# Kernel optimization log

Hardware: AMD Instinct MI355X
Metric: run time of the kernel (lower is better)

## Reference

```python
import jax, jax.numpy as jnp
import numpy as np

B, S, D = 2, 1024, 1024
L, E, F = 2, 8, 2048


def setup_inputs() -> dict:
    key = jax.random.key(0)
    kx, kp, k1, k2 = jax.random.split(key, 4)
    x = jax.random.normal(kx, (B, S, D), dtype=jnp.float32)
    # prototypes scaled so dot products are O(1), keeping softmax well-behaved
    protos = jax.random.normal(kp, (L, E, D), dtype=jnp.float32) / np.sqrt(D)
    W1 = jax.random.normal(k1, (L, E, D, F), dtype=jnp.float32) * 0.02
    W2 = jax.random.normal(k2, (L, E, F, D), dtype=jnp.float32) * 0.02
    return {"x": x, "protos": protos, "W1": W1, "W2": W2, "k": 2}


def _route(x, protos_l, k):
    # expert_mapping: abs(dot(prototype, input)) per expert, keep top-k, rest -> -inf, softmax
    scores = jnp.abs(jnp.einsum("bsd,ed->bse", x, protos_l))  # [B,S,E]
    topv, _ = jax.lax.top_k(scores, k)
    thresh = topv[..., -1:]  # k-th largest per token
    masked = jnp.where(scores >= thresh, scores, -jnp.inf)
    return jax.nn.softmax(masked, axis=-1)  # [B,S,E]


def reference(x, protos, W1, W2, k):
    n_layers = protos.shape[0]
    for l in range(n_layers):  # fixed small layer loop
        w = _route(x, protos[l], k)  # [B,S,E]
        h = jax.nn.relu(jnp.einsum("bsd,edf->bsef", x, W1[l]))  # [B,S,E,F]
        y = jnp.einsum("bsef,efd,bse->bsd", h, W2[l], w)  # weighted expert mix
        x = x + y
    return x
```

## Files before the change

### kernel.cpp

```cpp
#include <hip/hip_runtime.h>
#include <hip/hip_bf16.h>
#include <cstdint>

#define T_TOKENS 2048
#define DDIM 1024
#define FDIM 2048
#define NEXP 8
#define NLAYER 2
#define BMPAD 64
#define RMAX 4608
#define RALLOC 4736

#define ATILE_EL 2048
#define BTILE_EL 4096

typedef unsigned short u16;
typedef short bf16x8 __attribute__((ext_vector_type(8)));
typedef u16 u16x8 __attribute__((ext_vector_type(8)));
typedef u16 u16x4v __attribute__((ext_vector_type(4)));
typedef float f32x4 __attribute__((ext_vector_type(4)));

__device__ __forceinline__ u16 bf16_rn(float f) {
  unsigned u = __builtin_bit_cast(unsigned, f);
  u += 0x7fffu + ((u >> 16) & 1u);
  return (u16)(u >> 16);
}
__device__ __forceinline__ float bf16_f(u16 h) {
  unsigned u = ((unsigned)h) << 16;
  return __builtin_bit_cast(float, u);
}

__device__ __forceinline__ void gl16(const void* g, void* l) {
  __builtin_amdgcn_global_load_lds((const __attribute__((address_space(1))) void*)g,
                                   (__attribute__((address_space(3))) void*)l, 16, 0, 0);
}

__global__ __launch_bounds__(256) void route_kernel(
    const float* __restrict__ x, const float* __restrict__ protos,
    int* __restrict__ eid, float* __restrict__ wgt) {
  const int t = blockIdx.x;
  const int tid = threadIdx.x;
  const float* xr = x + (size_t)t * DDIM;
  __shared__ float red[NEXP][256];
  float acc[NEXP];
#pragma unroll
  for (int e = 0; e < NEXP; ++e) acc[e] = 0.f;
  for (int d = tid; d < DDIM; d += 256) {
    float xv = xr[d];
#pragma unroll
    for (int e = 0; e < NEXP; ++e) acc[e] += xv * protos[e * DDIM + d];
  }
#pragma unroll
  for (int e = 0; e < NEXP; ++e) red[e][tid] = acc[e];
  __syncthreads();
  for (int s = 128; s > 0; s >>= 1) {
    if (tid < s) {
#pragma unroll
      for (int e = 0; e < NEXP; ++e) red[e][tid] += red[e][tid + s];
    }
    __syncthreads();
  }
  if (tid == 0) {
    float m1 = -1.f, m2 = -1.f;
    int i1 = 0, i2 = 0;
#pragma unroll
    for (int e = 0; e < NEXP; ++e) {
      float s = fabsf(red[e][0]);
      if (s > m1) { m2 = m1; i2 = i1; m1 = s; i1 = e; }
      else if (s > m2) { m2 = s; i2 = e; }
    }
    float e2 = __expf(m2 - m1);
    float z = 1.f + e2;
    eid[t * 2] = i1;
    eid[t * 2 + 1] = i2;
    wgt[t * 2] = 1.f / z;
    wgt[t * 2 + 1] = e2 / z;
  }
}

__global__ __launch_bounds__(256) void compact_kernel(
    const int* __restrict__ eid, int* __restrict__ cnt, int* __restrict__ offp,
    int* __restrict__ row2token, int* __restrict__ pos) {
  __shared__ int lcnt[NEXP][256];
  __shared__ int s_off[NEXP], s_tot[NEXP];
  const int tid = threadIdx.x;
  const int base = tid * 16;

  int my[16];
#pragma unroll
  for (int i = 0; i < 4; ++i)
    *(int4*)&my[i * 4] = *(const int4*)(eid + base + i * 4);

#pragma unroll
  for (int e = 0; e < NEXP; ++e) {
    int c = 0;
#pragma unroll
    for (int i = 0; i < 16; ++i) c += (my[i] == e) ? 1 : 0;
    lcnt[e][tid] = c;
  }

  for (int r = tid; r < RMAX; r += 256) row2token[r] = -1;
  __syncthreads();

  if (tid < NEXP) {
    int run = 0;
    for (int i = 0; i < 256; ++i) {
      int v = lcnt[tid][i];
      lcnt[tid][i] = run;
      run += v;
    }
    s_tot[tid] = run;
  }
  __syncthreads();
  if (tid == 0) {
    int o = 0;
    for (int e = 0; e < NEXP; ++e) {
      s_off[e] = o;
      o += (s_tot[e] + BMPAD - 1) & ~(BMPAD - 1);
    }
  }
  __syncthreads();

  int myoff[NEXP];
#pragma unroll
  for (int e = 0; e < NEXP; ++e) myoff[e] = s_off[e] + lcnt[e][tid];
#pragma unroll
  for (int i = 0; i < 16; ++i) {
    int r = 0;
#pragma unroll
    for (int e = 0; e < NEXP; ++e) r = (my[i] == e) ? myoff[e] : r;
    row2token[r] = (base + i) >> 1;
    pos[base + i] = r;
#pragma unroll
    for (int e = 0; e < NEXP; ++e) myoff[e] += (my[i] == e) ? 1 : 0;
  }

  if (tid < NEXP) {
    cnt[tid] = s_tot[tid];
    offp[tid] = s_off[tid];
  }
}

__global__ __launch_bounds__(256) void gather_kernel(
    const float* __restrict__ x, const int* __restrict__ row2token,
    u16* __restrict__ Ahi, u16* __restrict__ Alo) {
  const int r = blockIdx.x;
  const int t = row2token[r];
  const int c = threadIdx.x * 4;
  float4 v = make_float4(0.f, 0.f, 0.f, 0.f);
  if (t >= 0) v = *(const float4*)(x + (size_t)t * DDIM + c);
  float vv[4] = {v.x, v.y, v.z, v.w};
  u16x4v hi, lo;
#pragma unroll
  for (int i = 0; i < 4; ++i) {
    u16 h = bf16_rn(vv[i]);
    hi[i] = h;
    lo[i] = bf16_rn(vv[i] - bf16_f(h));
  }
  const size_t el = ((size_t)(r >> 6) * (DDIM >> 5) + (c >> 5)) * ATILE_EL +
                    (size_t)(((c >> 3) & 3) * 64 + (r & 63)) * 8 + (c & 7);
  *(u16x4v*)(Ahi + el) = hi;
  *(u16x4v*)(Alo + el) = lo;
}

template <bool LO>
__global__ __launch_bounds__(256) void wconv_kernel(
    const float* __restrict__ W, u16* __restrict__ Hi, u16* __restrict__ Lo,
    int K, int N) {
  const int e = blockIdx.z, nb = blockIdx.x, kb = blockIdx.y;
  const float* Wp = W + ((size_t)e * K + (size_t)kb * 32) * N + nb * 128;
  __shared__ float tile[32][129];
  const int t = threadIdx.x;
#pragma unroll
  for (int i = 0; i < 4; ++i) {
    const int f4 = i * 256 + t;
    const int kr = f4 >> 5;
    const int c4 = (f4 & 31) * 4;
    float4 v = *(const float4*)(Wp + (size_t)kr * N + c4);
    *(float4*)&tile[kr][c4] = v;
  }
  __syncthreads();
  const size_t tb = (((size_t)e * (N >> 7) + nb) * (K >> 5) + kb) * BTILE_EL;
#pragma unroll
  for (int j = 0; j < 2; ++j) {
    const int cid = j * 256 + t;
    const int n = cid & 127, ksel = cid >> 7;
    u16x8 hv, lv;
#pragma unroll
    for (int i = 0; i < 8; ++i) {
      float f = tile[ksel * 8 + i][n];
      u16 h = bf16_rn(f);
      hv[i] = h;
      if (LO) lv[i] = bf16_rn(f - bf16_f(h));
    }
    *(u16x8*)(Hi + tb + (size_t)cid * 8) = hv;
    if (LO) *(u16x8*)(Lo + tb + (size_t)cid * 8) = lv;
  }
}

template <bool RELU, bool SPLIT, int OUTMODE, int SKF>
__global__ __launch_bounds__(256, SPLIT ? 2 : 4) void gemm_mfma(
    const u16* __restrict__ Ahi, const u16* __restrict__ Alo,
    const u16* __restrict__ Bhi, const u16* __restrict__ Blo,
    u16* __restrict__ OutHi, u16* __restrict__ OutLo, float* __restrict__ OutF,
    const int* __restrict__ cnt, const int* __restrict__ offp, int K, int N) {
  const int z = blockIdx.z;
  const int e = z / SKF, sk = z % SKF;
  const int cp = (cnt[e] + 63) & ~63;
  if ((int)(blockIdx.y * 128) >= cp) return;
  const int row0 = offp[e] + blockIdx.y * 128;
  const int rend = offp[e] + cp;
  const int n0 = blockIdx.x * 128;
  const int nkb = K >> 5;
  const int kbN = nkb / SKF;
  const int kb0 = sk * kbN;

  constexpr int BUF_EL = SPLIT ? 16384 : 8192;
  __shared__ u16 lds[2 * BUF_EL];

  const int tid = threadIdx.x;
  const int lane = tid & 63;
  const int wid = tid >> 6;
  const int wr = wid >> 1, wc = wid & 1;
  const int lr = lane & 15, kg = lane >> 4;
  const int lo16 = lane << 4;

  f32x4 acc[4][4];
#pragma unroll
  for (int i = 0; i < 4; ++i)
#pragma unroll
    for (int j = 0; j < 4; ++j)
#pragma unroll
      for (int r = 0; r < 4; ++r) acc[i][j][r] = 0.f;

  const int at0 = row0 >> 6;
  const size_t bbase = ((size_t)e * (N >> 7) + (n0 >> 7)) * nkb;

  auto STAGE = [&](int kb, int b) {
    char* d = (char*)(lds + b * BUF_EL);
    if constexpr (SPLIT) {
      if (wid == 0) {
#pragma unroll
        for (int t = 0; t < 2; ++t) {
          const char* g = (const char*)(Ahi + ((size_t)(at0 + t) * nkb + kb) * ATILE_EL);
#pragma unroll
          for (int i = 0; i < 4; ++i) gl16(g + i * 1024 + lo16, d + t * 4096 + i * 1024);
        }
      } else if (wid == 1) {
#pragma unroll
        for (int t = 0; t < 2; ++t) {
          const char* g = (const char*)(Alo + ((size_t)(at0 + t) * nkb + kb) * ATILE_EL);
#pragma unroll
          for (int i = 0; i < 4; ++i) gl16(g + i * 1024 + lo16, d + 8192 + t * 4096 + i * 1024);
        }
      } else if (wid == 2) {
        const char* g = (const char*)(Bhi + (bbase + kb) * BTILE_EL);
#pragma unroll
        for (int i = 0; i < 8; ++i) gl16(g + i * 1024 + lo16, d + 16384 + i * 1024);
      } else {
        const char* g = (const char*)(Blo + (bbase + kb) * BTILE_EL);
#pragma unroll
        for (int i = 0; i < 8; ++i) gl16(g + i * 1024 + lo16, d + 24576 + i * 1024);
      }
    } else {
      if (wid < 2) {
        const char* g = (const char*)(Ahi + ((size_t)(at0 + wid) * nkb + kb) * ATILE_EL);
#pragma unroll
        for (int i = 0; i < 4; ++i) gl16(g + i * 1024 + lo16, d + wid * 4096 + i * 1024);
      } else {
        const char* g = (const char*)(Bhi + (bbase + kb) * BTILE_EL) + (wid - 2) * 4096;
#pragma unroll
        for (int i = 0; i < 4; ++i) gl16(g + i * 1024 + lo16, d + 8192 + (wid - 2) * 4096 + i * 1024);
      }
    }
  };

  STAGE(kb0, 0);
  __syncthreads();

  int cur = 0;
  for (int kb = kb0; kb < kb0 + kbN; ++kb) {
    if (kb + 1 < kb0 + kbN) STAGE(kb + 1, cur ^ 1);

    const u16* buf = lds + cur * BUF_EL;
    const u16* AsH = buf + wr * 2048;
    const u16* BsH = buf + (SPLIT ? 8192 : 4096);
    const int arow = (kg * 64 + lr) * 8;
    const int bcol = (kg * 128 + wc * 64 + lr) * 8;

    bf16x8 ah[4], bh[4];
#pragma unroll
    for (int i = 0; i < 4; ++i) ah[i] = *(const bf16x8*)&AsH[arow + i * 128];
#pragma unroll
    for (int j = 0; j < 4; ++j) bh[j] = *(const bf16x8*)&BsH[bcol + j * 128];
#pragma unroll
    for (int i = 0; i < 4; ++i)
#pragma unroll
      for (int j = 0; j < 4; ++j)
        acc[i][j] = __builtin_amdgcn_mfma_f32_16x16x32_bf16(ah[i], bh[j], acc[i][j], 0, 0, 0);

    if constexpr (SPLIT) {
      const u16* AsL = buf + 4096 + wr * 2048;
      const u16* BsL = buf + 12288;
      bf16x8 bl[4];
#pragma unroll
      for (int j = 0; j < 4; ++j) bl[j] = *(const bf16x8*)&BsL[bcol + j * 128];
#pragma unroll
      for (int i = 0; i < 4; ++i)
#pragma unroll
        for (int j = 0; j < 4; ++j)
          acc[i][j] = __builtin_amdgcn_mfma_f32_16x16x32_bf16(ah[i], bl[j], acc[i][j], 0, 0, 0);
      bf16x8 al[4];
#pragma unroll
      for (int i = 0; i < 4; ++i) al[i] = *(const bf16x8*)&AsL[arow + i * 128];
#pragma unroll
      for (int i = 0; i < 4; ++i)
#pragma unroll
        for (int j = 0; j < 4; ++j)
          acc[i][j] = __builtin_amdgcn_mfma_f32_16x16x32_bf16(al[i], bh[j], acc[i][j], 0, 0, 0);
    }
    __syncthreads();
    cur ^= 1;
  }

  const int nkbO = N >> 5;
#pragma unroll
  for (int i = 0; i < 4; ++i) {
#pragma unroll
    for (int j = 0; j < 4; ++j) {
      const int Cj = n0 + wc * 64 + j * 16 + lr;
      f32x4 v = acc[i][j];
#pragma unroll
      for (int r = 0; r < 4; ++r) {
        const int R = row0 + wr * 64 + i * 16 + kg * 4 + r;
        if (R >= rend) continue;
        float f = v[r];
        if (RELU) f = fmaxf(f, 0.f);
        if constexpr (OUTMODE == 0) {
          OutF[((size_t)sk * RALLOC + R) * N + Cj] = f;
        } else {
          const size_t el = ((size_t)(R >> 6) * nkbO + (Cj >> 5)) * ATILE_EL +
                            (size_t)(((Cj >> 3) & 3) * 64 + (R & 63)) * 8 + (Cj & 7);
          u16 h = bf16_rn(f);
          OutHi[el] = h;
          if constexpr (OUTMODE == 1) OutLo[el] = bf16_rn(f - bf16_f(h));
        }
      }
    }
  }
}

__global__ __launch_bounds__(256) void apply_kernel(
    const float* __restrict__ part, const int* __restrict__ pos,
    const float* __restrict__ wgt, float* __restrict__ x) {
  const int t = blockIdx.x;
  const int c = threadIdx.x * 4;
  const int p0 = pos[t * 2], p1 = pos[t * 2 + 1];
  const float w0 = wgt[t * 2], w1 = wgt[t * 2 + 1];
  const float* P0 = part;
  const float* P1 = part + (size_t)RALLOC * DDIM;
  float4 xa = *(float4*)(x + (size_t)t * DDIM + c);
  const float4 a0 = *(const float4*)(P0 + (size_t)p0 * DDIM + c);
  const float4 b0 = *(const float4*)(P1 + (size_t)p0 * DDIM + c);
  const float4 a1 = *(const float4*)(P0 + (size_t)p1 * DDIM + c);
  const float4 b1 = *(const float4*)(P1 + (size_t)p1 * DDIM + c);
  xa.x += w0 * (a0.x + b0.x) + w1 * (a1.x + b1.x);
  xa.y += w0 * (a0.y + b0.y) + w1 * (a1.y + b1.y);
  xa.z += w0 * (a0.z + b0.z) + w1 * (a1.z + b1.z);
  xa.w += w0 * (a0.w + b0.w) + w1 * (a1.w + b1.w);
  *(float4*)(x + (size_t)t * DDIM + c) = xa;
}

extern "C" void kernel_launch(void* const* d_in, const int* in_sizes, int n_in,
                              void* d_out, int out_size, void* d_ws, size_t ws_size,
                              hipStream_t stream) {
  const float* x = (const float*)d_in[0];
  const float* protos = (const float*)d_in[1];
  const float* W1 = (const float*)d_in[2];
  const float* W2 = (const float*)d_in[3];
  float* xcur = (float*)d_out;

  u16* W_hi = (u16*)d_ws;
  u16* W_lo = W_hi + (size_t)NEXP * DDIM * FDIM;
  u16* Ag_hi = W_lo + (size_t)NEXP * DDIM * FDIM;
  u16* Ag_lo = Ag_hi + (size_t)RALLOC * DDIM;
  u16* h_hi = Ag_lo + (size_t)RALLOC * DDIM;
  u16* h_lo = h_hi + (size_t)RALLOC * FDIM;
  float* part = (float*)(h_lo + (size_t)RALLOC * FDIM);
  float* wgt = part + (size_t)2 * RALLOC * DDIM;
  int* eid = (int*)(wgt + T_TOKENS * 2);
  int* pos = eid + T_TOKENS * 2;
  int* cnt = pos + T_TOKENS * 2;
  int* offp = cnt + NEXP;
  int* row2token = offp + NEXP;

  hipMemcpyAsync(xcur, x, (size_t)T_TOKENS * DDIM * sizeof(float),
                 hipMemcpyDeviceToDevice, stream);

  for (int l = 0; l < NLAYER; ++l) {
    route_kernel<<<T_TOKENS, 256, 0, stream>>>(
        xcur, protos + (size_t)l * NEXP * DDIM, eid, wgt);
    compact_kernel<<<1, 256, 0, stream>>>(eid, cnt, offp, row2token, pos);
    gather_kernel<<<RMAX, 256, 0, stream>>>(xcur, row2token, Ag_hi, Ag_lo);
    const float* W1l = W1 + (size_t)l * NEXP * DDIM * FDIM;
    const float* W2l = W2 + (size_t)l * NEXP * FDIM * DDIM;
    if (l == 0) {
      wconv_kernel<true><<<dim3(FDIM / 128, DDIM / 32, NEXP), 256, 0, stream>>>(
          W1l, W_hi, W_lo, DDIM, FDIM);
      gemm_mfma<true, true, 1, 1><<<dim3(FDIM / 128, RMAX / 128, NEXP), 256, 0, stream>>>(
          Ag_hi, Ag_lo, W_hi, W_lo, h_hi, h_lo, nullptr, cnt, offp, DDIM, FDIM);
      wconv_kernel<true><<<dim3(DDIM / 128, FDIM / 32, NEXP), 256, 0, stream>>>(
          W2l, W_hi, W_lo, FDIM, DDIM);
      gemm_mfma<false, true, 0, 2><<<dim3(DDIM / 128, RMAX / 128, NEXP * 2), 256, 0, stream>>>(
          h_hi, h_lo, W_hi, W_lo, nullptr, nullptr, part, cnt, offp, FDIM, DDIM);
    } else {
      wconv_kernel<false><<<dim3(FDIM / 128, DDIM / 32, NEXP), 256, 0, stream>>>(
          W1l, W_hi, nullptr, DDIM, FDIM);
      gemm_mfma<true, false, 2, 1><<<dim3(FDIM / 128, RMAX / 128, NEXP), 256, 0, stream>>>(
          Ag_hi, nullptr, W_hi, nullptr, h_hi, nullptr, nullptr, cnt, offp, DDIM, FDIM);
      wconv_kernel<false><<<dim3(DDIM / 128, FDIM / 32, NEXP), 256, 0, stream>>>(
          W2l, W_hi, nullptr, FDIM, DDIM);
      gemm_mfma<false, false, 0, 2><<<dim3(DDIM / 128, RMAX / 128, NEXP * 2), 256, 0, stream>>>(
          h_hi, nullptr, W_hi, nullptr, nullptr, nullptr, part, cnt, offp, FDIM, DDIM);
    }
    apply_kernel<<<T_TOKENS, 256, 0, stream>>>(part, pos, wgt, xcur);
  }
}
```

Measured before the change: 392.9 us.

## Split GEMM into 64-row split-precision and plain kernels with XCD swizzle

Splits the templated GEMM into two kernels. The split-precision (hi/lo bf16) layer-0 kernel now uses 64-row tiles with occupancy 3 and no split-K, and its partial-sum apply reads a single buffer. Both GEMMs remap block IDs with an XCD-aware swizzle so neighbouring tiles share L2, and the routing kernel is vectorised with float4 loads. Smaller tiles raise parallelism and drop the split-K second partial buffer, at the cost of more B-tile reloads per output.

```diff
diff --git a/kernel.cpp b/kernel.cpp
--- a/kernel.cpp
+++ b/kernel.cpp
@@ -35,20 +35,31 @@
                                    (__attribute__((address_space(3))) void*)l, 16, 0, 0);
 }
 
+__device__ __forceinline__ void xcd_swizzle(int& bx, int& by, int& bz) {
+  const unsigned gx = gridDim.x, gy = gridDim.y;
+  const unsigned lin = blockIdx.x + gx * (blockIdx.y + gy * blockIdx.z);
+  const unsigned nwg = gx * gy * gridDim.z;
+  const unsigned nl = (lin & 7u) * (nwg >> 3) + (lin >> 3);
+  bx = nl % gx;
+  const unsigned t = nl / gx;
+  by = t % gy;
+  bz = t / gy;
+}
+
 __global__ __launch_bounds__(256) void route_kernel(
     const float* __restrict__ x, const float* __restrict__ protos,
     int* __restrict__ eid, float* __restrict__ wgt) {
   const int t = blockIdx.x;
   const int tid = threadIdx.x;
-  const float* xr = x + (size_t)t * DDIM;
+  const float4* xr4 = (const float4*)(x + (size_t)t * DDIM);
+  const float4* pr4 = (const float4*)protos;
   __shared__ float red[NEXP][256];
+  const float4 xv = xr4[tid];
   float acc[NEXP];
 #pragma unroll
-  for (int e = 0; e < NEXP; ++e) acc[e] = 0.f;
-  for (int d = tid; d < DDIM; d += 256) {
-    float xv = xr[d];
-#pragma unroll
-    for (int e = 0; e < NEXP; ++e) acc[e] += xv * protos[e * DDIM + d];
+  for (int e = 0; e < NEXP; ++e) {
+    const float4 p = pr4[e * 256 + tid];
+    acc[e] = xv.x * p.x + xv.y * p.y + xv.z * p.z + xv.w * p.w;
   }
 #pragma unroll
   for (int e = 0; e < NEXP; ++e) red[e][tid] = acc[e];
@@ -198,24 +209,22 @@
   }
 }
 
-template <bool RELU, bool SPLIT, int OUTMODE, int SKF>
-__global__ __launch_bounds__(256, SPLIT ? 2 : 4) void gemm_mfma(
+template <bool RELU, int OUTMODE>
+__global__ __launch_bounds__(256, 3) void gemm_split(
     const u16* __restrict__ Ahi, const u16* __restrict__ Alo,
     const u16* __restrict__ Bhi, const u16* __restrict__ Blo,
     u16* __restrict__ OutHi, u16* __restrict__ OutLo, float* __restrict__ OutF,
     const int* __restrict__ cnt, const int* __restrict__ offp, int K, int N) {
-  const int z = blockIdx.z;
-  const int e = z / SKF, sk = z % SKF;
+  int bx, by, bz;
+  xcd_swizzle(bx, by, bz);
+  const int e = bz;
   const int cp = (cnt[e] + 63) & ~63;
-  if ((int)(blockIdx.y * 128) >= cp) return;
-  const int row0 = offp[e] + blockIdx.y * 128;
-  const int rend = offp[e] + cp;
-  const int n0 = blockIdx.x * 128;
+  if (by * 64 >= cp) return;
+  const int row0 = offp[e] + by * 64;
+  const int n0 = bx * 128;
   const int nkb = K >> 5;
-  const int kbN = nkb / SKF;
-  const int kb0 = sk * kbN;
-
-  constexpr int BUF_EL = SPLIT ? 16384 : 8192;
+
+  constexpr int BUF_EL = 12288;
   __shared__ u16 lds[2 * BUF_EL];
 
   const int tid = threadIdx.x;
@@ -225,6 +234,129 @@
   const int lr = lane & 15, kg = lane >> 4;
   const int lo16 = lane << 4;
 
+  f32x4 acc[2][4];
+#pragma unroll
+  for (int i = 0; i < 2; ++i)
+#pragma unroll
+    for (int j = 0; j < 4; ++j)
+#pragma unroll
+      for (int r = 0; r < 4; ++r) acc[i][j][r] = 0.f;
+
+  const size_t abase = (size_t)(row0 >> 6) * nkb;
+  const size_t bbase = ((size_t)e * (N >> 7) + (n0 >> 7)) * nkb;
+
+  auto STAGE = [&](int kb, int b) {
+    char* d = (char*)(lds + b * BUF_EL);
+    if (wid == 0) {
+      const char* gh = (const char*)(Ahi + (abase + kb) * ATILE_EL);
+      const char* gl = (const char*)(Alo + (abase + kb) * ATILE_EL);
+#pragma unroll
+      for (int i = 0; i < 4; ++i) gl16(gh + i * 1024 + lo16, d + i * 1024);
+#pragma unroll
+      for (int i = 0; i < 4; ++i) gl16(gl + i * 1024 + lo16, d + 4096 + i * 1024);
+    } else if (wid == 1) {
+      const char* g = (const char*)(Bhi + (bbase + kb) * BTILE_EL);
+#pragma unroll
+      for (int i = 0; i < 8; ++i) gl16(g + i * 1024 + lo16, d + 8192 + i * 1024);
+    } else if (wid == 2) {
+      const char* g = (const char*)(Blo + (bbase + kb) * BTILE_EL);
+#pragma unroll
+      for (int i = 0; i < 8; ++i) gl16(g + i * 1024 + lo16, d + 16384 + i * 1024);
+    }
+  };
+
+  STAGE(0, 0);
+  __syncthreads();
+
+  int cur = 0;
+  for (int kb = 0; kb < nkb; ++kb) {
+    if (kb + 1 < nkb) STAGE(kb + 1, cur ^ 1);
+
+    const u16* buf = lds + cur * BUF_EL;
+    const u16* AsH = buf;
+    const u16* AsL = buf + 2048;
+    const u16* BsH = buf + 4096;
+    const u16* BsL = buf + 8192;
+    const int arow = (kg * 64 + wr * 32 + lr) * 8;
+    const int bcol = (kg * 128 + wc * 64 + lr) * 8;
+
+    bf16x8 ah0 = *(const bf16x8*)&AsH[arow];
+    bf16x8 ah1 = *(const bf16x8*)&AsH[arow + 128];
+    bf16x8 bh[4];
+#pragma unroll
+    for (int j = 0; j < 4; ++j) bh[j] = *(const bf16x8*)&BsH[bcol + j * 128];
+#pragma unroll
+    for (int j = 0; j < 4; ++j) {
+      acc[0][j] = __builtin_amdgcn_mfma_f32_16x16x32_bf16(ah0, bh[j], acc[0][j], 0, 0, 0);
+      acc[1][j] = __builtin_amdgcn_mfma_f32_16x16x32_bf16(ah1, bh[j], acc[1][j], 0, 0, 0);
+    }
+    bf16x8 al0 = *(const bf16x8*)&AsL[arow];
+    bf16x8 al1 = *(const bf16x8*)&AsL[arow + 128];
+#pragma unroll
+    for (int j = 0; j < 4; ++j) {
+      bf16x8 bl = *(const bf16x8*)&BsL[bcol + j * 128];
+      acc[0][j] = __builtin_amdgcn_mfma_f32_16x16x32_bf16(ah0, bl, acc[0][j], 0, 0, 0);
+      acc[1][j] = __builtin_amdgcn_mfma_f32_16x16x32_bf16(ah1, bl, acc[1][j], 0, 0, 0);
+      acc[0][j] = __builtin_amdgcn_mfma_f32_16x16x32_bf16(al0, bh[j], acc[0][j], 0, 0, 0);
+      acc[1][j] = __builtin_amdgcn_mfma_f32_16x16x32_bf16(al1, bh[j], acc[1][j], 0, 0, 0);
+    }
+    __syncthreads();
+    cur ^= 1;
+  }
+
+  const int nkbO = N >> 5;
+#pragma unroll
+  for (int i = 0; i < 2; ++i) {
+#pragma unroll
+    for (int j = 0; j < 4; ++j) {
+      const int Cj = n0 + wc * 64 + j * 16 + lr;
+      f32x4 v = acc[i][j];
+#pragma unroll
+      for (int r = 0; r < 4; ++r) {
+        const int R = row0 + wr * 32 + i * 16 + kg * 4 + r;
+        float f = v[r];
+        if (RELU) f = fmaxf(f, 0.f);
+        if constexpr (OUTMODE == 0) {
+          OutF[(size_t)R * N + Cj] = f;
+        } else {
+          const size_t el = ((size_t)(R >> 6) * nkbO + (Cj >> 5)) * ATILE_EL +
+                            (size_t)(((Cj >> 3) & 3) * 64 + (R & 63)) * 8 + (Cj & 7);
+          u16 h = bf16_rn(f);
+          OutHi[el] = h;
+          OutLo[el] = bf16_rn(f - bf16_f(h));
+        }
+      }
+    }
+  }
+}
+
+template <bool RELU, int OUTMODE, int SKF>
+__global__ __launch_bounds__(256, 4) void gemm_plain(
+    const u16* __restrict__ Ahi, const u16* __restrict__ Bhi,
+    u16* __restrict__ OutHi, float* __restrict__ OutF,
+    const int* __restrict__ cnt, const int* __restrict__ offp, int K, int N) {
+  int bx, by, bz;
+  xcd_swizzle(bx, by, bz);
+  const int e = bz / SKF, sk = bz % SKF;
+  const int cp = (cnt[e] + 63) & ~63;
+  if (by * 128 >= cp) return;
+  const int row0 = offp[e] + by * 128;
+  const int rend = offp[e] + cp;
+  const int n0 = bx * 128;
+  const int nkb = K >> 5;
+  const int kbN = nkb / SKF;
+  const int kb0 = sk * kbN;
+
+  constexpr int BUF_EL = 8192;
+  __shared__ u16 lds[2 * BUF_EL];
+
+  const int tid = threadIdx.x;
+  const int lane = tid & 63;
+  const int wid = tid >> 6;
+  const int wr = wid >> 1, wc = wid & 1;
+  const int lr = lane & 15, kg = lane >> 4;
+  const int lo16 = lane << 4;
+
   f32x4 acc[4][4];
 #pragma unroll
   for (int i = 0; i < 4; ++i)
@@ -238,40 +370,14 @@
 
   auto STAGE = [&](int kb, int b) {
     char* d = (char*)(lds + b * BUF_EL);
-    if constexpr (SPLIT) {
-      if (wid == 0) {
-#pragma unroll
-        for (int t = 0; t < 2; ++t) {
-          const char* g = (const char*)(Ahi + ((size_t)(at0 + t) * nkb + kb) * ATILE_EL);
-#pragma unroll
-          for (int i = 0; i < 4; ++i) gl16(g + i * 1024 + lo16, d + t * 4096 + i * 1024);
-        }
-      } else if (wid == 1) {
-#pragma unroll
-        for (int t = 0; t < 2; ++t) {
-          const char* g = (const char*)(Alo + ((size_t)(at0 + t) * nkb + kb) * ATILE_EL);
-#pragma unroll
-          for (int i = 0; i < 4; ++i) gl16(g + i * 1024 + lo16, d + 8192 + t * 4096 + i * 1024);
-        }
-      } else if (wid == 2) {
-        const char* g = (const char*)(Bhi + (bbase + kb) * BTILE_EL);
-#pragma unroll
-        for (int i = 0; i < 8; ++i) gl16(g + i * 1024 + lo16, d + 16384 + i * 1024);
-      } else {
-        const char* g = (const char*)(Blo + (bbase + kb) * BTILE_EL);
-#pragma unroll
-        for (int i = 0; i < 8; ++i) gl16(g + i * 1024 + lo16, d + 24576 + i * 1024);
-      }
+    if (wid < 2) {
+      const char* g = (const char*)(Ahi + ((size_t)(at0 + wid) * nkb + kb) * ATILE_EL);
+#pragma unroll
+      for (int i = 0; i < 4; ++i) gl16(g + i * 1024 + lo16, d + wid * 4096 + i * 1024);
     } else {
-      if (wid < 2) {
-        const char* g = (const char*)(Ahi + ((size_t)(at0 + wid) * nkb + kb) * ATILE_EL);
-#pragma unroll
-        for (int i = 0; i < 4; ++i) gl16(g + i * 1024 + lo16, d + wid * 4096 + i * 1024);
-      } else {
-        const char* g = (const char*)(Bhi + (bbase + kb) * BTILE_EL) + (wid - 2) * 4096;
-#pragma unroll
-        for (int i = 0; i < 4; ++i) gl16(g + i * 1024 + lo16, d + 8192 + (wid - 2) * 4096 + i * 1024);
-      }
+      const char* g = (const char*)(Bhi + (bbase + kb) * BTILE_EL) + (wid - 2) * 4096;
+#pragma unroll
+      for (int i = 0; i < 4; ++i) gl16(g + i * 1024 + lo16, d + 8192 + (wid - 2) * 4096 + i * 1024);
     }
   };
 
@@ -284,7 +390,7 @@
 
     const u16* buf = lds + cur * BUF_EL;
     const u16* AsH = buf + wr * 2048;
-    const u16* BsH = buf + (SPLIT ? 8192 : 4096);
+    const u16* BsH = buf + 4096;
     const int arow = (kg * 64 + lr) * 8;
     const int bcol = (kg * 128 + wc * 64 + lr) * 8;
 
@@ -298,27 +404,6 @@
 #pragma unroll
       for (int j = 0; j < 4; ++j)
         acc[i][j] = __builtin_amdgcn_mfma_f32_16x16x32_bf16(ah[i], bh[j], acc[i][j], 0, 0, 0);
-
-    if constexpr (SPLIT) {
-      const u16* AsL = buf + 4096 + wr * 2048;
-      const u16* BsL = buf + 12288;
-      bf16x8 bl[4];
-#pragma unroll
-      for (int j = 0; j < 4; ++j) bl[j] = *(const bf16x8*)&BsL[bcol + j * 128];
-#pragma unroll
-      for (int i = 0; i < 4; ++i)
-#pragma unroll
-        for (int j = 0; j < 4; ++j)
-          acc[i][j] = __builtin_amdgcn_mfma_f32_16x16x32_bf16(ah[i], bl[j], acc[i][j], 0, 0, 0);
-      bf16x8 al[4];
-#pragma unroll
-      for (int i = 0; i < 4; ++i) al[i] = *(const bf16x8*)&AsL[arow + i * 128];
-#pragma unroll
-      for (int i = 0; i < 4; ++i)
-#pragma unroll
-        for (int j = 0; j < 4; ++j)
-          acc[i][j] = __builtin_amdgcn_mfma_f32_16x16x32_bf16(al[i], bh[j], acc[i][j], 0, 0, 0);
-    }
     __syncthreads();
     cur ^= 1;
   }
@@ -341,15 +426,14 @@
         } else {
           const size_t el = ((size_t)(R >> 6) * nkbO + (Cj >> 5)) * ATILE_EL +
                             (size_t)(((Cj >> 3) & 3) * 64 + (R & 63)) * 8 + (Cj & 7);
-          u16 h = bf16_rn(f);
-          OutHi[el] = h;
-          if constexpr (OUTMODE == 1) OutLo[el] = bf16_rn(f - bf16_f(h));
+          OutHi[el] = bf16_rn(f);
         }
       }
     }
   }
 }
 
+template <int NPART>
 __global__ __launch_bounds__(256) void apply_kernel(
     const float* __restrict__ part, const int* __restrict__ pos,
     const float* __restrict__ wgt, float* __restrict__ x) {
@@ -357,17 +441,20 @@
   const int c = threadIdx.x * 4;
   const int p0 = pos[t * 2], p1 = pos[t * 2 + 1];
   const float w0 = wgt[t * 2], w1 = wgt[t * 2 + 1];
-  const float* P0 = part;
-  const float* P1 = part + (size_t)RALLOC * DDIM;
   float4 xa = *(float4*)(x + (size_t)t * DDIM + c);
-  const float4 a0 = *(const float4*)(P0 + (size_t)p0 * DDIM + c);
-  const float4 b0 = *(const float4*)(P1 + (size_t)p0 * DDIM + c);
-  const float4 a1 = *(const float4*)(P0 + (size_t)p1 * DDIM + c);
-  const float4 b1 = *(const float4*)(P1 + (size_t)p1 * DDIM + c);
-  xa.x += w0 * (a0.x + b0.x) + w1 * (a1.x + b1.x);
-  xa.y += w0 * (a0.y + b0.y) + w1 * (a1.y + b1.y);
-  xa.z += w0 * (a0.z + b0.z) + w1 * (a1.z + b1.z);
-  xa.w += w0 * (a0.w + b0.w) + w1 * (a1.w + b1.w);
+  float4 y0 = *(const float4*)(part + (size_t)p0 * DDIM + c);
+  float4 y1 = *(const float4*)(part + (size_t)p1 * DDIM + c);
+  if (NPART == 2) {
+    const float* P1 = part + (size_t)RALLOC * DDIM;
+    const float4 b0 = *(const float4*)(P1 + (size_t)p0 * DDIM + c);
+    const float4 b1 = *(const float4*)(P1 + (size_t)p1 * DDIM + c);
+    y0.x += b0.x; y0.y += b0.y; y0.z += b0.z; y0.w += b0.w;
+    y1.x += b1.x; y1.y += b1.y; y1.z += b1.z; y1.w += b1.w;
+  }
+  xa.x += w0 * y0.x + w1 * y1.x;
+  xa.y += w0 * y0.y + w1 * y1.y;
+  xa.z += w0 * y0.z + w1 * y1.z;
+  xa.w += w0 * y0.w + w1 * y1.w;
   *(float4*)(x + (size_t)t * DDIM + c) = xa;
 }
 
@@ -407,22 +494,23 @@
     if (l == 0) {
       wconv_kernel<true><<<dim3(FDIM / 128, DDIM / 32, NEXP), 256, 0, stream>>>(
           W1l, W_hi, W_lo, DDIM, FDIM);
-      gemm_mfma<true, true, 1, 1><<<dim3(FDIM / 128, RMAX / 128, NEXP), 256, 0, stream>>>(
+      gemm_split<true, 1><<<dim3(FDIM / 128, RMAX / 64, NEXP), 256, 0, stream>>>(
           Ag_hi, Ag_lo, W_hi, W_lo, h_hi, h_lo, nullptr, cnt, offp, DDIM, FDIM);
       wconv_kernel<true><<<dim3(DDIM / 128, FDIM / 32, NEXP), 256, 0, stream>>>(
           W2l, W_hi, W_lo, FDIM, DDIM);
-      gemm_mfma<false, true, 0, 2><<<dim3(DDIM / 128, RMAX / 128, NEXP * 2), 256, 0, stream>>>(
+      gemm_split<false, 0><<<dim3(DDIM / 128, RMAX / 64, NEXP), 256, 0, stream>>>(
           h_hi, h_lo, W_hi, W_lo, nullptr, nullptr, part, cnt, offp, FDIM, DDIM);
+      apply_kernel<1><<<T_TOKENS, 256, 0, stream>>>(part, pos, wgt, xcur);
     } else {
       wconv_kernel<false><<<dim3(FDIM / 128, DDIM / 32, NEXP), 256, 0, stream>>>(
           W1l, W_hi, nullptr, DDIM, FDIM);
-      gemm_mfma<true, false, 2, 1><<<dim3(FDIM / 128, RMAX / 128, NEXP), 256, 0, stream>>>(
-          Ag_hi, nullptr, W_hi, nullptr, h_hi, nullptr, nullptr, cnt, offp, DDIM, FDIM);
+      gemm_plain<true, 2, 1><<<dim3(FDIM / 128, RMAX / 128, NEXP), 256, 0, stream>>>(
+          Ag_hi, W_hi, h_hi, nullptr, cnt, offp, DDIM, FDIM);
       wconv_kernel<false><<<dim3(DDIM / 128, FDIM / 32, NEXP), 256, 0, stream>>>(
           W2l, W_hi, nullptr, FDIM, DDIM);
-      gemm_mfma<false, false, 0, 2><<<dim3(DDIM / 128, RMAX / 128, NEXP * 2), 256, 0, stream>>>(
-          h_hi, nullptr, W_hi, nullptr, nullptr, nullptr, part, cnt, offp, FDIM, DDIM);
-    }
-    apply_kernel<<<T_TOKENS, 256, 0, stream>>>(part, pos, wgt, xcur);
-  }
-}
+      gemm_plain<false, 0, 2><<<dim3(DDIM / 128, RMAX / 128, NEXP * 2), 256, 0, stream>>>(
+          h_hi, W_hi, nullptr, part, cnt, offp, FDIM, DDIM);
+      apply_kernel<2><<<T_TOKENS, 256, 0, stream>>>(part, pos, wgt, xcur);
+    }
+  }
+}
```

New measurement: 371.8 us. 1.06x faster.
